# Performance work log

Measured on AMD Instinct MI355X. Metric: run time of the kernel, lower is better.

The kernel has to match this reference:

```python
import jax, jax.numpy as jnp
import numpy as np

B, IN, HS, NM = 256, 512, 512, 1

def setup_inputs() -> dict:
    key = jax.random.key(0)
    ks = jax.random.split(key, 12)
    def kaiming(k, shape):
        fan_in = shape[0]
        bound = float(np.sqrt(6.0 / fan_in))  # kaiming_uniform with a=sqrt(5) approx; use gain sqrt(2): bound = sqrt(6/fan_in)
        return jax.random.uniform(k, shape, jnp.float32, -bound, bound)
    return {
        "x_t":  jax.random.normal(ks[0], (B, IN), jnp.float32),
        "h_t":  jax.random.normal(ks[1], (B, HS), jnp.float32),
        "c_t":  jax.random.normal(ks[2], (B, HS), jnp.float32),
        "hebb": jax.random.normal(ks[3], (B, HS, HS), jnp.float32) * 0.1,
        "W":    kaiming(ks[4], (IN, 4 * HS)),
        "U":    kaiming(ks[5], (HS, 4 * HS)),
        "bias": jnp.zeros((4 * HS,), jnp.float32),
        "alpha": jax.random.normal(ks[6], (1, 1, HS), jnp.float32) * 1e-4,
        "nm_w": jax.random.normal(ks[7], (NM, HS), jnp.float32),
        "nm_b": jnp.zeros((NM,), jnp.float32),
        "mt_w": jax.random.normal(ks[8], (HS, NM), jnp.float32),
        "mt_b": jnp.zeros((HS,), jnp.float32),
    }

def reference(x_t, h_t, c_t, hebb, W, U, bias, alpha, nm_w, nm_b, mt_w, mt_b):
    # g_t_hebb = h_t (B,1,HS) @ (alpha*hebb) (B,HS,HS) -> (B,HS)
    g_t_hebb = jnp.einsum('bh,bhk->bk', h_t, alpha * hebb)
    gates = x_t @ W + h_t @ U + bias                        # (B, 4*HS)
    i_t = jax.nn.sigmoid(gates[:, :HS])
    f_t = jax.nn.sigmoid(gates[:, HS:2 * HS])
    g_t = jnp.tanh(gates[:, 2 * HS:3 * HS] + g_t_hebb)
    o_t = jax.nn.sigmoid(gates[:, 3 * HS:])
    # rank-1 outer product per batch element: (B,HS,1)@(B,1,HS)
    delta_hebb = jnp.einsum('bi,bj->bij', h_t, g_t)         # (B,HS,HS)
    m_t = jnp.tanh(h_t @ nm_w.T + nm_b)                     # (B,NM)
    m_t = m_t @ mt_w.T + mt_b                               # (B,HS)
    hebb_new = jnp.clip(hebb + m_t[:, None, :] * delta_hebb, -2.0, 2.0)
    c_new = f_t * c_t + i_t * g_t
    h_new = o_t * jnp.tanh(c_new)
    return h_new, c_new, hebb_new
```

## Files before the change

### kernel.cpp

```cpp
#include <hip/hip_runtime.h>
#include <math.h>


__device__ __forceinline__ float sigm(float x) { return 1.0f / (1.0f + __expf(-x)); }
__device__ __forceinline__ float tanh_fast(float x) { return 1.0f - 2.0f / (1.0f + __expf(2.0f * x)); }
__device__ __forceinline__ float clip2(float v) { return fminf(fmaxf(v, -2.0f), 2.0f); }

__global__ __launch_bounds__(256, 4)
void gates_gemm(const float* __restrict__ x, const float* __restrict__ h,
                const float* __restrict__ W, const float* __restrict__ U,
                const float* __restrict__ bias, float* __restrict__ gates)
{
    __shared__ float As[64][64];
    __shared__ float Bs[64][40];

    const int t     = threadIdx.x;
    const int bcol0 = blockIdx.x * 32;
    const int brow0 = blockIdx.y * 64;
    const int row   = t & 63;
    const int cg    = t >> 6;

    float acc[8] = {};

    for (int ks = 0; ks < 16; ++ks) {
        const float* srcA;
        const float* srcB;
        int ka;
        if (ks < 8) { srcA = x; srcB = W; ka = ks * 64; }
        else        { srcA = h; srcB = U; ka = ks * 64 - 512; }

        float4 av[4];
        #pragma unroll
        for (int m = 0; m < 4; ++m)
            av[m] = *(const float4*)&srcA[(size_t)(brow0 + row) * 512 + ka + cg * 16 + m * 4];
        const int kr0 = t >> 3;
        const int c4  = t & 7;
        float4 bv0 = *(const float4*)&srcB[(size_t)(ka + kr0)      * 2048 + bcol0 + c4 * 4];
        float4 bv1 = *(const float4*)&srcB[(size_t)(ka + kr0 + 32) * 2048 + bcol0 + c4 * 4];

        __syncthreads();
        #pragma unroll
        for (int m = 0; m < 4; ++m) {
            As[cg * 16 + m * 4 + 0][row] = av[m].x;
            As[cg * 16 + m * 4 + 1][row] = av[m].y;
            As[cg * 16 + m * 4 + 2][row] = av[m].z;
            As[cg * 16 + m * 4 + 3][row] = av[m].w;
        }
        *(float4*)&Bs[kr0][c4 * 4]      = bv0;
        *(float4*)&Bs[kr0 + 32][c4 * 4] = bv1;
        __syncthreads();

        #pragma unroll
        for (int k = 0; k < 64; ++k) {
            const float a = As[k][row];
            const float4 b0 = *(const float4*)&Bs[k][cg * 8];
            const float4 b1 = *(const float4*)&Bs[k][cg * 8 + 4];
            acc[0] += a * b0.x; acc[1] += a * b0.y; acc[2] += a * b0.z; acc[3] += a * b0.w;
            acc[4] += a * b1.x; acc[5] += a * b1.y; acc[6] += a * b1.z; acc[7] += a * b1.w;
        }
    }

    const int colb = bcol0 + cg * 8;
    float4 o0, o1;
    o0.x = acc[0] + bias[colb + 0]; o0.y = acc[1] + bias[colb + 1];
    o0.z = acc[2] + bias[colb + 2]; o0.w = acc[3] + bias[colb + 3];
    o1.x = acc[4] + bias[colb + 4]; o1.y = acc[5] + bias[colb + 5];
    o1.z = acc[6] + bias[colb + 6]; o1.w = acc[7] + bias[colb + 7];
    float* gp = &gates[(size_t)(brow0 + row) * 2048 + colb];
    *(float4*)gp       = o0;
    *(float4*)(gp + 4) = o1;
}

__global__ __launch_bounds__(512, 8)
void hebb_fused(const float* __restrict__ h_t, const float* __restrict__ c_t,
                const float* __restrict__ hebb, const float* __restrict__ alpha,
                const float* __restrict__ nm_w, const float* __restrict__ nm_b,
                const float* __restrict__ mt_w, const float* __restrict__ mt_b,
                const float* __restrict__ gates, float* __restrict__ out)
{
    const int b   = blockIdx.x >> 4;
    const int jt  = blockIdx.x & 15;
    const int t   = threadIdx.x;
    const int tj4 = t & 7;
    const int ti  = t >> 3;

    __shared__ __align__(16) float hsh[512];
    __shared__ float redm[512];
    __shared__ __align__(16) float red[64][36];
    __shared__ __align__(16) float upd[32];
    __shared__ float msh;

    const float hv0 = h_t[(size_t)b * 512 + t];
    const float nw  = nm_w[t];

    const float4* hb    = (const float4*)(hebb + (size_t)b * 262144);
    const int     cbase = jt * 8 + tj4;
    float4 r[8];
    #pragma unroll
    for (int k = 0; k < 8; ++k)
        r[k] = hb[(size_t)(ti * 8 + k) * 128 + cbase];

    hsh[t]  = hv0;
    redm[t] = hv0 * nw;
    __syncthreads();

    if (t < 64) {
        float v = 0.f;
        #pragma unroll
        for (int q = 0; q < 8; ++q) v += redm[t + q * 64];
        #pragma unroll
        for (int off = 32; off > 0; off >>= 1) v += __shfl_down(v, off);
        if (t == 0) msh = tanh_fast(v + nm_b[0]);
    }

    float4 ps = {0.f, 0.f, 0.f, 0.f};
    #pragma unroll
    for (int k = 0; k < 8; ++k) {
        const float hv = hsh[ti * 8 + k];
        ps.x += hv * r[k].x;
        ps.y += hv * r[k].y;
        ps.z += hv * r[k].z;
        ps.w += hv * r[k].w;
    }
    *(float4*)&red[ti][tj4 * 4] = ps;
    __syncthreads();

    if (t < 64) {
        const int c  = t & 31;
        const int hf = t >> 5;
        float s = 0.f;
        #pragma unroll
        for (int q = 0; q < 32; ++q) s += red[hf * 32 + q][c];
        s += __shfl_xor(s, 32);
        if (hf == 0) {
            const int j = jt * 32 + c;
            const size_t gb = (size_t)b * 2048;
            const float g  = tanh_fast(gates[gb + 1024 + j] + alpha[j] * s);
            const float mm = msh * mt_w[j] + mt_b[j];
            upd[c] = mm * g;
            const float it_ = sigm(gates[gb + j]);
            const float ft  = sigm(gates[gb + 512 + j]);
            const float ot  = sigm(gates[gb + 1536 + j]);
            const float cn  = ft * c_t[(size_t)b * 512 + j] + it_ * g;
            out[(size_t)b * 512 + j]          = ot * tanh_fast(cn);
            out[131072 + (size_t)b * 512 + j] = cn;
        }
    }
    __syncthreads();

    const float4 u = *(const float4*)&upd[tj4 * 4];
    float4* ho = (float4*)(out + 262144 + (size_t)b * 262144);
    #pragma unroll
    for (int k = 0; k < 8; ++k) {
        const float hv = hsh[ti * 8 + k];
        float4 w;
        w.x = clip2(r[k].x + u.x * hv);
        w.y = clip2(r[k].y + u.y * hv);
        w.z = clip2(r[k].z + u.z * hv);
        w.w = clip2(r[k].w + u.w * hv);
        ho[(size_t)(ti * 8 + k) * 128 + cbase] = w;
    }
}

extern "C" void kernel_launch(void* const* d_in, const int* in_sizes, int n_in,
                              void* d_out, int out_size, void* d_ws, size_t ws_size,
                              hipStream_t stream)
{
    const float* x_t   = (const float*)d_in[0];
    const float* h_t   = (const float*)d_in[1];
    const float* c_t   = (const float*)d_in[2];
    const float* hebb  = (const float*)d_in[3];
    const float* W     = (const float*)d_in[4];
    const float* U     = (const float*)d_in[5];
    const float* bias  = (const float*)d_in[6];
    const float* alpha = (const float*)d_in[7];
    const float* nm_w  = (const float*)d_in[8];
    const float* nm_b  = (const float*)d_in[9];
    const float* mt_w  = (const float*)d_in[10];
    const float* mt_b  = (const float*)d_in[11];
    float* out   = (float*)d_out;
    float* gates = (float*)d_ws;

    dim3 g1(64, 4);
    gates_gemm<<<g1, 256, 0, stream>>>(x_t, h_t, W, U, bias, gates);
    hebb_fused<<<4096, 512, 0, stream>>>(h_t, c_t, hebb, alpha, nm_w, nm_b,
                                         mt_w, mt_b, gates, out);
}
```

Baseline: 512.1 us.

## Fuse gates GEMM into hebb kernel as per-block GEMV

Removes the separate gates GEMM kernel and its workspace round trip. Each hebb block now computes its own 128 gate columns for one batch row as a GEMV over W and U. The block index is reordered so the batch index varies fastest, letting blocks that share weight columns run close together and hit in L2. The cost is that the weights are re-read for every batch row instead of once per tile, which greatly increases cache and memory read traffic. Each block also does a long serial 256-step dot product per thread before its hebb work can finish.

```diff
diff --git a/kernel.cpp b/kernel.cpp
--- a/kernel.cpp
+++ b/kernel.cpp
@@ -6,92 +6,29 @@
 __device__ __forceinline__ float tanh_fast(float x) { return 1.0f - 2.0f / (1.0f + __expf(2.0f * x)); }
 __device__ __forceinline__ float clip2(float v) { return fminf(fmaxf(v, -2.0f), 2.0f); }
 
-__global__ __launch_bounds__(256, 4)
-void gates_gemm(const float* __restrict__ x, const float* __restrict__ h,
-                const float* __restrict__ W, const float* __restrict__ U,
-                const float* __restrict__ bias, float* __restrict__ gates)
+__global__ __launch_bounds__(512, 6)
+void nm_lstm_fused(const float* __restrict__ x_t, const float* __restrict__ h_t,
+                   const float* __restrict__ c_t, const float* __restrict__ hebb,
+                   const float* __restrict__ W, const float* __restrict__ U,
+                   const float* __restrict__ bias, const float* __restrict__ alpha,
+                   const float* __restrict__ nm_w, const float* __restrict__ nm_b,
+                   const float* __restrict__ mt_w, const float* __restrict__ mt_b,
+                   float* __restrict__ out)
 {
-    __shared__ float As[64][64];
-    __shared__ float Bs[64][40];
-
-    const int t     = threadIdx.x;
-    const int bcol0 = blockIdx.x * 32;
-    const int brow0 = blockIdx.y * 64;
-    const int row   = t & 63;
-    const int cg    = t >> 6;
-
-    float acc[8] = {};
-
-    for (int ks = 0; ks < 16; ++ks) {
-        const float* srcA;
-        const float* srcB;
-        int ka;
-        if (ks < 8) { srcA = x; srcB = W; ka = ks * 64; }
-        else        { srcA = h; srcB = U; ka = ks * 64 - 512; }
-
-        float4 av[4];
-        #pragma unroll
-        for (int m = 0; m < 4; ++m)
-            av[m] = *(const float4*)&srcA[(size_t)(brow0 + row) * 512 + ka + cg * 16 + m * 4];
-        const int kr0 = t >> 3;
-        const int c4  = t & 7;
-        float4 bv0 = *(const float4*)&srcB[(size_t)(ka + kr0)      * 2048 + bcol0 + c4 * 4];
-        float4 bv1 = *(const float4*)&srcB[(size_t)(ka + kr0 + 32) * 2048 + bcol0 + c4 * 4];
-
-        __syncthreads();
-        #pragma unroll
-        for (int m = 0; m < 4; ++m) {
-            As[cg * 16 + m * 4 + 0][row] = av[m].x;
-            As[cg * 16 + m * 4 + 1][row] = av[m].y;
-            As[cg * 16 + m * 4 + 2][row] = av[m].z;
-            As[cg * 16 + m * 4 + 3][row] = av[m].w;
-        }
-        *(float4*)&Bs[kr0][c4 * 4]      = bv0;
-        *(float4*)&Bs[kr0 + 32][c4 * 4] = bv1;
-        __syncthreads();
-
-        #pragma unroll
-        for (int k = 0; k < 64; ++k) {
-            const float a = As[k][row];
-            const float4 b0 = *(const float4*)&Bs[k][cg * 8];
-            const float4 b1 = *(const float4*)&Bs[k][cg * 8 + 4];
-            acc[0] += a * b0.x; acc[1] += a * b0.y; acc[2] += a * b0.z; acc[3] += a * b0.w;
-            acc[4] += a * b1.x; acc[5] += a * b1.y; acc[6] += a * b1.z; acc[7] += a * b1.w;
-        }
-    }
-
-    const int colb = bcol0 + cg * 8;
-    float4 o0, o1;
-    o0.x = acc[0] + bias[colb + 0]; o0.y = acc[1] + bias[colb + 1];
-    o0.z = acc[2] + bias[colb + 2]; o0.w = acc[3] + bias[colb + 3];
-    o1.x = acc[4] + bias[colb + 4]; o1.y = acc[5] + bias[colb + 5];
-    o1.z = acc[6] + bias[colb + 6]; o1.w = acc[7] + bias[colb + 7];
-    float* gp = &gates[(size_t)(brow0 + row) * 2048 + colb];
-    *(float4*)gp       = o0;
-    *(float4*)(gp + 4) = o1;
-}
-
-__global__ __launch_bounds__(512, 8)
-void hebb_fused(const float* __restrict__ h_t, const float* __restrict__ c_t,
-                const float* __restrict__ hebb, const float* __restrict__ alpha,
-                const float* __restrict__ nm_w, const float* __restrict__ nm_b,
-                const float* __restrict__ mt_w, const float* __restrict__ mt_b,
-                const float* __restrict__ gates, float* __restrict__ out)
-{
-    const int b   = blockIdx.x >> 4;
-    const int jt  = blockIdx.x & 15;
-    const int t   = threadIdx.x;
+    const int bx = blockIdx.x;
+    const int jt = bx >> 8;
+    const int b  = bx & 255;
+    const int t  = threadIdx.x;
     const int tj4 = t & 7;
     const int ti  = t >> 3;
 
-    __shared__ __align__(16) float hsh[512];
+    __shared__ __align__(16) float xh[1024];
     __shared__ float redm[512];
     __shared__ __align__(16) float red[64][36];
+    __shared__ float gred[4][128];
+    __shared__ float gsh[128];
     __shared__ __align__(16) float upd[32];
     __shared__ float msh;
-
-    const float hv0 = h_t[(size_t)b * 512 + t];
-    const float nw  = nm_w[t];
 
     const float4* hb    = (const float4*)(hebb + (size_t)b * 262144);
     const int     cbase = jt * 8 + tj4;
@@ -100,23 +37,44 @@
     for (int k = 0; k < 8; ++k)
         r[k] = hb[(size_t)(ti * 8 + k) * 128 + cbase];
 
-    hsh[t]  = hv0;
-    redm[t] = hv0 * nw;
+    const float xv  = x_t[(size_t)b * 512 + t];
+    const float hv0 = h_t[(size_t)b * 512 + t];
+    xh[t]       = xv;
+    xh[512 + t] = hv0;
+    redm[t]     = hv0 * nm_w[t];
     __syncthreads();
+
+    const int o    = t & 127;
+    const int q    = t >> 7;
+    const int gcol = (o >> 5) * 512 + jt * 32 + (o & 31);
+    const float* Bp = (q < 2) ? (W + (size_t)(q * 256) * 2048 + gcol)
+                              : (U + (size_t)((q - 2) * 256) * 2048 + gcol);
+    const float* xp = &xh[q * 256];
+    float acc = 0.f;
+    #pragma unroll 4
+    for (int k = 0; k < 256; ++k)
+        acc += xp[k] * Bp[(size_t)k * 2048];
+    gred[q][o] = acc;
 
     if (t < 64) {
         float v = 0.f;
         #pragma unroll
-        for (int q = 0; q < 8; ++q) v += redm[t + q * 64];
+        for (int qq = 0; qq < 8; ++qq) v += redm[t + qq * 64];
         #pragma unroll
         for (int off = 32; off > 0; off >>= 1) v += __shfl_down(v, off);
         if (t == 0) msh = tanh_fast(v + nm_b[0]);
+    }
+    __syncthreads();
+
+    if (t < 128) {
+        const int gc = (t >> 5) * 512 + jt * 32 + (t & 31);
+        gsh[t] = gred[0][t] + gred[1][t] + gred[2][t] + gred[3][t] + bias[gc];
     }
 
     float4 ps = {0.f, 0.f, 0.f, 0.f};
     #pragma unroll
     for (int k = 0; k < 8; ++k) {
-        const float hv = hsh[ti * 8 + k];
+        const float hv = xh[512 + ti * 8 + k];
         ps.x += hv * r[k].x;
         ps.y += hv * r[k].y;
         ps.z += hv * r[k].z;
@@ -130,17 +88,16 @@
         const int hf = t >> 5;
         float s = 0.f;
         #pragma unroll
-        for (int q = 0; q < 32; ++q) s += red[hf * 32 + q][c];
+        for (int qq = 0; qq < 32; ++qq) s += red[hf * 32 + qq][c];
         s += __shfl_xor(s, 32);
         if (hf == 0) {
             const int j = jt * 32 + c;
-            const size_t gb = (size_t)b * 2048;
-            const float g  = tanh_fast(gates[gb + 1024 + j] + alpha[j] * s);
+            const float g  = tanh_fast(gsh[64 + c] + alpha[j] * s);
             const float mm = msh * mt_w[j] + mt_b[j];
             upd[c] = mm * g;
-            const float it_ = sigm(gates[gb + j]);
-            const float ft  = sigm(gates[gb + 512 + j]);
-            const float ot  = sigm(gates[gb + 1536 + j]);
+            const float it_ = sigm(gsh[c]);
+            const float ft  = sigm(gsh[32 + c]);
+            const float ot  = sigm(gsh[96 + c]);
             const float cn  = ft * c_t[(size_t)b * 512 + j] + it_ * g;
             out[(size_t)b * 512 + j]          = ot * tanh_fast(cn);
             out[131072 + (size_t)b * 512 + j] = cn;
@@ -152,7 +109,7 @@
     float4* ho = (float4*)(out + 262144 + (size_t)b * 262144);
     #pragma unroll
     for (int k = 0; k < 8; ++k) {
-        const float hv = hsh[ti * 8 + k];
+        const float hv = xh[512 + ti * 8 + k];
         float4 w;
         w.x = clip2(r[k].x + u.x * hv);
         w.y = clip2(r[k].y + u.y * hv);
@@ -178,11 +135,8 @@
     const float* nm_b  = (const float*)d_in[9];
     const float* mt_w  = (const float*)d_in[10];
     const float* mt_b  = (const float*)d_in[11];
-    float* out   = (float*)d_out;
-    float* gates = (float*)d_ws;
+    float* out = (float*)d_out;
 
-    dim3 g1(64, 4);
-    gates_gemm<<<g1, 256, 0, stream>>>(x_t, h_t, W, U, bias, gates);
-    hebb_fused<<<4096, 512, 0, stream>>>(h_t, c_t, hebb, alpha, nm_w, nm_b,
-                                         mt_w, mt_b, gates, out);
+    nm_lstm_fused<<<4096, 512, 0, stream>>>(x_t, h_t, c_t, hebb, W, U, bias,
+                                            alpha, nm_w, nm_b, mt_w, mt_b, out);
 }
```

Measured after the change: 641.6 us. 25.3% more time.

## Process four column tiles per block with register double-buffered hebb loads

Applied to the files above, without the earlier changes.

The hebb kernel now handles four 32-column tiles per block, so it launches a quarter as many blocks. Each iteration prefetches the next tile's hebb values into a second register set while the current tile is reduced and updated. This amortises the h load, the neuromodulator reduction and block launch cost, and overlaps memory loads with compute. The trade-off is higher register use, with launch bounds lowered to 4, fewer blocks to spread across CUs, and extra barriers per block.

```diff
diff --git a/kernel.cpp b/kernel.cpp
--- a/kernel.cpp
+++ b/kernel.cpp
@@ -71,37 +71,39 @@
     *(float4*)(gp + 4) = o1;
 }
 
-__global__ __launch_bounds__(512, 8)
+__global__ __launch_bounds__(512, 4)
 void hebb_fused(const float* __restrict__ h_t, const float* __restrict__ c_t,
                 const float* __restrict__ hebb, const float* __restrict__ alpha,
                 const float* __restrict__ nm_w, const float* __restrict__ nm_b,
                 const float* __restrict__ mt_w, const float* __restrict__ mt_b,
                 const float* __restrict__ gates, float* __restrict__ out)
 {
-    const int b   = blockIdx.x >> 4;
-    const int jt  = blockIdx.x & 15;
+    const int p   = blockIdx.x;
+    const int b   = p >> 2;
+    const int jt0 = (p & 3) * 4;
     const int t   = threadIdx.x;
     const int tj4 = t & 7;
     const int ti  = t >> 3;
-
-    __shared__ __align__(16) float hsh[512];
+    const int rbase = ti * 8;
+
+    __shared__ float hsh[512];
     __shared__ float redm[512];
     __shared__ __align__(16) float red[64][36];
     __shared__ __align__(16) float upd[32];
     __shared__ float msh;
 
-    const float hv0 = h_t[(size_t)b * 512 + t];
-    const float nw  = nm_w[t];
-
-    const float4* hb    = (const float4*)(hebb + (size_t)b * 262144);
-    const int     cbase = jt * 8 + tj4;
-    float4 r[8];
+    const float4* hb = (const float4*)(hebb + (size_t)b * 262144);
+    float4*       ho = (float4*)(out + 262144 + (size_t)b * 262144);
+
+    float4 A[8], Bv[8];
+    const int cb0 = jt0 * 8 + tj4;
     #pragma unroll
     for (int k = 0; k < 8; ++k)
-        r[k] = hb[(size_t)(ti * 8 + k) * 128 + cbase];
-
+        A[k] = hb[(size_t)(rbase + k) * 128 + cb0];
+
+    const float hv0 = h_t[(size_t)b * 512 + t];
     hsh[t]  = hv0;
-    redm[t] = hv0 * nw;
+    redm[t] = hv0 * nm_w[t];
     __syncthreads();
 
     if (t < 64) {
@@ -113,52 +115,68 @@
         if (t == 0) msh = tanh_fast(v + nm_b[0]);
     }
 
-    float4 ps = {0.f, 0.f, 0.f, 0.f};
+    float hrow[8];
     #pragma unroll
-    for (int k = 0; k < 8; ++k) {
-        const float hv = hsh[ti * 8 + k];
-        ps.x += hv * r[k].x;
-        ps.y += hv * r[k].y;
-        ps.z += hv * r[k].z;
-        ps.w += hv * r[k].w;
-    }
-    *(float4*)&red[ti][tj4 * 4] = ps;
-    __syncthreads();
-
-    if (t < 64) {
-        const int c  = t & 31;
-        const int hf = t >> 5;
-        float s = 0.f;
-        #pragma unroll
-        for (int q = 0; q < 32; ++q) s += red[hf * 32 + q][c];
-        s += __shfl_xor(s, 32);
-        if (hf == 0) {
-            const int j = jt * 32 + c;
-            const size_t gb = (size_t)b * 2048;
-            const float g  = tanh_fast(gates[gb + 1024 + j] + alpha[j] * s);
-            const float mm = msh * mt_w[j] + mt_b[j];
-            upd[c] = mm * g;
-            const float it_ = sigm(gates[gb + j]);
-            const float ft  = sigm(gates[gb + 512 + j]);
-            const float ot  = sigm(gates[gb + 1536 + j]);
-            const float cn  = ft * c_t[(size_t)b * 512 + j] + it_ * g;
-            out[(size_t)b * 512 + j]          = ot * tanh_fast(cn);
-            out[131072 + (size_t)b * 512 + j] = cn;
-        }
-    }
-    __syncthreads();
-
-    const float4 u = *(const float4*)&upd[tj4 * 4];
-    float4* ho = (float4*)(out + 262144 + (size_t)b * 262144);
+    for (int k = 0; k < 8; ++k) hrow[k] = hsh[rbase + k];
+
+    const size_t gb = (size_t)b * 2048;
+
     #pragma unroll
-    for (int k = 0; k < 8; ++k) {
-        const float hv = hsh[ti * 8 + k];
-        float4 w;
-        w.x = clip2(r[k].x + u.x * hv);
-        w.y = clip2(r[k].y + u.y * hv);
-        w.z = clip2(r[k].z + u.z * hv);
-        w.w = clip2(r[k].w + u.w * hv);
-        ho[(size_t)(ti * 8 + k) * 128 + cbase] = w;
+    for (int i = 0; i < 4; ++i) {
+        float4* cur = (i & 1) ? Bv : A;
+        float4* nxt = (i & 1) ? A  : Bv;
+
+        if (i < 3) {
+            const int cbn = (jt0 + i + 1) * 8 + tj4;
+            #pragma unroll
+            for (int k = 0; k < 8; ++k)
+                nxt[k] = hb[(size_t)(rbase + k) * 128 + cbn];
+        }
+
+        float4 ps = {0.f, 0.f, 0.f, 0.f};
+        #pragma unroll
+        for (int k = 0; k < 8; ++k) {
+            ps.x += hrow[k] * cur[k].x;
+            ps.y += hrow[k] * cur[k].y;
+            ps.z += hrow[k] * cur[k].z;
+            ps.w += hrow[k] * cur[k].w;
+        }
+        *(float4*)&red[ti][tj4 * 4] = ps;
+        __syncthreads();
+
+        if (t < 64) {
+            const int c  = t & 31;
+            const int hf = t >> 5;
+            float s = 0.f;
+            #pragma unroll
+            for (int q = 0; q < 32; ++q) s += red[hf * 32 + q][c];
+            s += __shfl_xor(s, 32);
+            if (hf == 0) {
+                const int j = (jt0 + i) * 32 + c;
+                const float g  = tanh_fast(gates[gb + 1024 + j] + alpha[j] * s);
+                const float mm = msh * mt_w[j] + mt_b[j];
+                upd[c] = mm * g;
+                const float it_ = sigm(gates[gb + j]);
+                const float ft  = sigm(gates[gb + 512 + j]);
+                const float ot  = sigm(gates[gb + 1536 + j]);
+                const float cn  = ft * c_t[(size_t)b * 512 + j] + it_ * g;
+                out[(size_t)b * 512 + j]          = ot * tanh_fast(cn);
+                out[131072 + (size_t)b * 512 + j] = cn;
+            }
+        }
+        __syncthreads();
+
+        const float4 u  = *(const float4*)&upd[tj4 * 4];
+        const int   cbi = (jt0 + i) * 8 + tj4;
+        #pragma unroll
+        for (int k = 0; k < 8; ++k) {
+            float4 w;
+            w.x = clip2(cur[k].x + u.x * hrow[k]);
+            w.y = clip2(cur[k].y + u.y * hrow[k]);
+            w.z = clip2(cur[k].z + u.z * hrow[k]);
+            w.w = clip2(cur[k].w + u.w * hrow[k]);
+            ho[(size_t)(rbase + k) * 128 + cbi] = w;
+        }
     }
 }
 
@@ -183,6 +201,6 @@
 
     dim3 g1(64, 4);
     gates_gemm<<<g1, 256, 0, stream>>>(x_t, h_t, W, U, bias, gates);
-    hebb_fused<<<4096, 512, 0, stream>>>(h_t, c_t, hebb, alpha, nm_w, nm_b,
+    hebb_fused<<<1024, 512, 0, stream>>>(h_t, c_t, hebb, alpha, nm_w, nm_b,
                                          mt_w, mt_b, gates, out);
 }
```

Result: no change. 507.8 us (-0.8%).
